# Kernel tuning notes

Measured on AMD Instinct MI355X. Metric: run time of the kernel, lower is better.

The kernel has to match this reference:

```python
import jax, jax.numpy as jnp
import numpy as np

# Problem sizes: batch(+heads), seq (m=n), head dim, nonzeros per row
B, M, N, K, R = 8, 4096, 4096, 64, 128
NNZ = M * R


def setup_inputs() -> dict:
    key = jax.random.key(0)
    k1, k2, k3, k4 = jax.random.split(key, 4)
    # Uniform CSR: R nonzeros per row, columns sorted within each row.
    row_offsets = jnp.arange(M + 1, dtype=jnp.int32) * R
    column_indices = jax.random.randint(k4, (M, R), 0, N, dtype=jnp.int32)
    column_indices = jnp.sort(column_indices, axis=1).reshape(NNZ)
    # diffsort(row_offsets): row ids sorted by descending row length (load balancing,
    # does not affect the math).
    diffs = row_offsets[1:] - row_offsets[:-1]
    row_indices = jnp.argsort(-diffs).astype(jnp.int32)
    q3d = jax.random.normal(k1, (B, M, K), dtype=jnp.float32)
    k3d = jax.random.normal(k2, (B, N, K), dtype=jnp.float32)
    v3d = jax.random.normal(k3, (B, N, K), dtype=jnp.float32)
    # `values` is only an output buffer for sddmm in the original; contents unused.
    values = jnp.zeros((B, NNZ), dtype=jnp.float32)
    return {
        "row_indices": row_indices,
        "row_offsets": row_offsets,
        "column_indices": column_indices,
        "q3d": q3d,
        "k3d": k3d,
        "v3d": v3d,
        "values": values,
    }


def reference(row_indices, row_offsets, column_indices, q3d, k3d, v3d, values):
    m = row_offsets.shape[0] - 1
    nnz = column_indices.shape[0]
    # Row id of each CSR nonzero.
    row_ids = jnp.searchsorted(
        row_offsets, jnp.arange(nnz, dtype=row_offsets.dtype), side="right"
    ) - 1
    cols = column_indices

    # SDDMM: logits[b, e] = <Q[b, row(e), :], K[b, col(e), :]>  -> [B, nnz]
    logits = jnp.einsum("bed,bed->be", q3d[:, row_ids, :], k3d[:, cols, :])

    def attend_one(lg_b, v_b):
        # Sparse per-row softmax over the nonzeros of each row.
        mx = jax.ops.segment_max(lg_b, row_ids, num_segments=m)
        ex = jnp.exp(lg_b - mx[row_ids])
        den = jax.ops.segment_sum(ex, row_ids, num_segments=m)
        w = ex / den[row_ids]  # [nnz]
        # SPMM: out[i, :] = sum_{e in row i} w[e] * V[col(e), :]
        return jax.ops.segment_sum(w[:, None] * v_b[cols, :], row_ids, num_segments=m)

    return jax.vmap(attend_one)(logits, v3d)  # [B, M, K]
```

## Files before the change

### kernel.cpp

```cpp
#include <hip/hip_runtime.h>

#define Bc 8
#define Mc 4096
#define Nc 4096
#define Kc 64
#define Rc 128

typedef _Float16 h16;
typedef h16 h16x2 __attribute__((ext_vector_type(2)));
typedef h16 h16x4 __attribute__((ext_vector_type(4)));
typedef h16 h16x8 __attribute__((ext_vector_type(8)));

__global__ __launch_bounds__(256) void cvt_fp16(
    const float4* __restrict__ K4, const float4* __restrict__ V4,
    h16x4* __restrict__ Kh4, h16x4* __restrict__ Vh4)
{
    const int n4 = Bc * Nc * Kc / 4;
    int i = blockIdx.x * 256 + threadIdx.x;
    const float4* src; h16x4* dst; int idx;
    if (i < n4) { src = K4; dst = Kh4; idx = i; }
    else        { src = V4; dst = Vh4; idx = i - n4; }
    float4 v = src[idx];
    h16x4 o = { (h16)v.x, (h16)v.y, (h16)v.z, (h16)v.w };
    dst[idx] = o;
}

__global__ __launch_bounds__(256) void sattn_kernel(
    const int* __restrict__ cols,
    const float* __restrict__ Q,
    const h16* __restrict__ Kh,
    const h16* __restrict__ Vh,
    float* __restrict__ out)
{
    const int b   = blockIdx.x & 7;
    const int row = blockIdx.x >> 3;
    const int t   = threadIdx.x;
    const int g   = t >> 3;
    const int ln  = t & 7;

    __shared__ float s_w[Rc];
    __shared__ __align__(16) float s_part[32][Kc];
    __shared__ __align__(16) float s_red[4][Kc];
    __shared__ float s_invden;

    int col4[4];
    #pragma unroll
    for (int p = 0; p < 4; ++p) col4[p] = cols[row * Rc + p * 32 + g];

    const float4* qp = (const float4*)(Q + (((unsigned)b * Mc + row) << 6) + ln * 8);
    float4 q0 = qp[0], q1 = qp[1];
    h16x2 qh[4];
    qh[0] = h16x2{ (h16)q0.x, (h16)q0.y };
    qh[1] = h16x2{ (h16)q0.z, (h16)q0.w };
    qh[2] = h16x2{ (h16)q1.x, (h16)q1.y };
    qh[3] = h16x2{ (h16)q1.z, (h16)q1.w };

    h16x8 kv[4];
    #pragma unroll
    for (int p = 0; p < 4; ++p)
        kv[p] = *(const h16x8*)(Kh + ((((unsigned)b * Nc + col4[p]) << 6) + ln * 8));

    #pragma unroll
    for (int p = 0; p < 4; ++p) {
        float acc = 0.f;
        #pragma unroll
        for (int j = 0; j < 4; ++j) {
            h16x2 kj = { kv[p][2 * j], kv[p][2 * j + 1] };
#if defined(__has_builtin)
#if __has_builtin(__builtin_amdgcn_fdot2)
            acc = __builtin_amdgcn_fdot2(qh[j], kj, acc, false);
#else
            acc += (float)qh[j].x * (float)kj.x + (float)qh[j].y * (float)kj.y;
#endif
#else
            acc += (float)qh[j].x * (float)kj.x + (float)qh[j].y * (float)kj.y;
#endif
        }
        acc += __shfl_xor(acc, 1, 64);
        acc += __shfl_xor(acc, 2, 64);
        acc += __shfl_xor(acc, 4, 64);
        if (ln == 0) s_w[p * 32 + g] = acc;
    }

    h16x8 vv[4];
    #pragma unroll
    for (int p = 0; p < 4; ++p)
        vv[p] = *(const h16x8*)(Vh + ((((unsigned)b * Nc + col4[p]) << 6) + ln * 8));

    __syncthreads();

    if (t < 64) {
        float l0 = s_w[t], l1 = s_w[t + 64];
        float m = fmaxf(l0, l1);
        #pragma unroll
        for (int o = 32; o; o >>= 1) m = fmaxf(m, __shfl_xor(m, o, 64));
        float e0 = __expf(l0 - m), e1 = __expf(l1 - m);
        s_w[t] = e0; s_w[t + 64] = e1;
        float s = e0 + e1;
        #pragma unroll
        for (int o = 32; o; o >>= 1) s += __shfl_xor(s, o, 64);
        if (t == 0) s_invden = 1.0f / s;
    }
    __syncthreads();

    float acc8[8] = {0.f,0.f,0.f,0.f,0.f,0.f,0.f,0.f};
    #pragma unroll
    for (int p = 0; p < 4; ++p) {
        const float w = s_w[p * 32 + g];
        #pragma unroll
        for (int j = 0; j < 8; ++j)
            acc8[j] = fmaf((float)vv[p][j], w, acc8[j]);
    }
    *(float4*)&s_part[g][ln * 8]     = *(float4*)&acc8[0];
    *(float4*)&s_part[g][ln * 8 + 4] = *(float4*)&acc8[4];
    __syncthreads();

    {
        const int k = t & 63, qq = t >> 6;
        float r = 0.f;
        #pragma unroll
        for (int j = 0; j < 8; ++j) r += s_part[qq * 8 + j][k];
        s_red[qq][k] = r;
    }
    __syncthreads();
    if (t < 64) {
        float r = (s_red[0][t] + s_red[1][t]) + (s_red[2][t] + s_red[3][t]);
        out[(((unsigned)b * Mc + row) << 6) + t] = r * s_invden;
    }
}

extern "C" void kernel_launch(void* const* d_in, const int* in_sizes, int n_in,
                              void* d_out, int out_size, void* d_ws, size_t ws_size,
                              hipStream_t stream) {
    const int*   cols = (const int*)d_in[2];
    const float* Q    = (const float*)d_in[3];
    const float* Km   = (const float*)d_in[4];
    const float* Vm   = (const float*)d_in[5];
    float* out = (float*)d_out;

    h16* Kh = (h16*)d_ws;
    h16* Vh = Kh + (size_t)Bc * Nc * Kc;

    const int n4 = Bc * Nc * Kc / 4;
    cvt_fp16<<<dim3(2 * n4 / 256), dim3(256), 0, stream>>>(
        (const float4*)Km, (const float4*)Vm, (h16x4*)Kh, (h16x4*)Vh);
    sattn_kernel<<<dim3(Bc * Mc), dim3(256), 0, stream>>>(cols, Q, Kh, Vh, out);
}
```

Measured before the change: 148.0 us.

## Process one row per wavefront and drop shared-memory reductions

Result: slower. 154.1 us (+4.1%).

```diff
diff --git a/kernel.cpp b/kernel.cpp
--- a/kernel.cpp
+++ b/kernel.cpp
@@ -10,122 +10,123 @@
 typedef h16 h16x2 __attribute__((ext_vector_type(2)));
 typedef h16 h16x4 __attribute__((ext_vector_type(4)));
 typedef h16 h16x8 __attribute__((ext_vector_type(8)));
+typedef float f32x4 __attribute__((ext_vector_type(4)));
 
 __global__ __launch_bounds__(256) void cvt_fp16(
-    const float4* __restrict__ K4, const float4* __restrict__ V4,
-    h16x4* __restrict__ Kh4, h16x4* __restrict__ Vh4)
+    const f32x4* __restrict__ K4, const f32x4* __restrict__ V4,
+    const f32x4* __restrict__ Q4,
+    h16x4* __restrict__ Kh4, h16x4* __restrict__ Vh4, h16x4* __restrict__ Qh4)
 {
-    const int n4 = Bc * Nc * Kc / 4;
-    int i = blockIdx.x * 256 + threadIdx.x;
-    const float4* src; h16x4* dst; int idx;
-    if (i < n4) { src = K4; dst = Kh4; idx = i; }
-    else        { src = V4; dst = Vh4; idx = i - n4; }
-    float4 v = src[idx];
+    const int nb4   = Nc * Kc / 4;
+    const int b     = blockIdx.x & 7;
+    const int chunk = blockIdx.x >> 3;
+    const int tsel  = chunk >> 8;
+    const int idx   = b * nb4 + ((chunk & 255) << 8) + threadIdx.x;
+    const f32x4* src = (tsel == 0) ? K4 : (tsel == 1) ? V4 : Q4;
+    h16x4*       dst = (tsel == 0) ? Kh4 : (tsel == 1) ? Vh4 : Qh4;
+    f32x4 v = __builtin_nontemporal_load(&src[idx]);
     h16x4 o = { (h16)v.x, (h16)v.y, (h16)v.z, (h16)v.w };
     dst[idx] = o;
 }
 
-__global__ __launch_bounds__(256) void sattn_kernel(
+__global__ __launch_bounds__(256, 4) void sattn_kernel(
     const int* __restrict__ cols,
-    const float* __restrict__ Q,
+    const h16* __restrict__ Qh,
     const h16* __restrict__ Kh,
     const h16* __restrict__ Vh,
     float* __restrict__ out)
 {
     const int b   = blockIdx.x & 7;
-    const int row = blockIdx.x >> 3;
-    const int t   = threadIdx.x;
-    const int g   = t >> 3;
-    const int ln  = t & 7;
+    const int w   = threadIdx.x >> 6;
+    const int row = ((blockIdx.x >> 3) << 2) | w;
+    const int l   = threadIdx.x & 63;
+    const int g   = l >> 3;
+    const int ln  = l & 7;
 
-    __shared__ float s_w[Rc];
-    __shared__ __align__(16) float s_part[32][Kc];
-    __shared__ __align__(16) float s_red[4][Kc];
-    __shared__ float s_invden;
+    const h16* Kb = Kh + ((size_t)b * Nc) * Kc;
+    const h16* Vb = Vh + ((size_t)b * Nc) * Kc;
 
-    int col4[4];
+    h16x8 qv = __builtin_nontemporal_load(
+        (const h16x8*)(Qh + (((size_t)b * Mc + row) << 6) + ln * 8));
+
+    const int* crow = cols + row * Rc;
+    int col16[16];
     #pragma unroll
-    for (int p = 0; p < 4; ++p) col4[p] = cols[row * Rc + p * 32 + g];
+    for (int p = 0; p < 16; ++p)
+        col16[p] = __builtin_nontemporal_load(&crow[p * 8 + g]);
 
-    const float4* qp = (const float4*)(Q + (((unsigned)b * Mc + row) << 6) + ln * 8);
-    float4 q0 = qp[0], q1 = qp[1];
-    h16x2 qh[4];
-    qh[0] = h16x2{ (h16)q0.x, (h16)q0.y };
-    qh[1] = h16x2{ (h16)q0.z, (h16)q0.w };
-    qh[2] = h16x2{ (h16)q1.x, (h16)q1.y };
-    qh[3] = h16x2{ (h16)q1.z, (h16)q1.w };
+    h16x8 kv[16];
+    #pragma unroll
+    for (int p = 0; p < 16; ++p)
+        kv[p] = *(const h16x8*)(Kb + (((unsigned)col16[p]) << 6) + ln * 8);
 
-    h16x8 kv[4];
+    float lg[16];
     #pragma unroll
-    for (int p = 0; p < 4; ++p)
-        kv[p] = *(const h16x8*)(Kh + ((((unsigned)b * Nc + col4[p]) << 6) + ln * 8));
-
-    #pragma unroll
-    for (int p = 0; p < 4; ++p) {
+    for (int p = 0; p < 16; ++p) {
         float acc = 0.f;
         #pragma unroll
         for (int j = 0; j < 4; ++j) {
+            h16x2 qj = { qv[2 * j], qv[2 * j + 1] };
             h16x2 kj = { kv[p][2 * j], kv[p][2 * j + 1] };
 #if defined(__has_builtin)
 #if __has_builtin(__builtin_amdgcn_fdot2)
-            acc = __builtin_amdgcn_fdot2(qh[j], kj, acc, false);
+            acc = __builtin_amdgcn_fdot2(qj, kj, acc, false);
 #else
-            acc += (float)qh[j].x * (float)kj.x + (float)qh[j].y * (float)kj.y;
+            acc += (float)qj.x * (float)kj.x + (float)qj.y * (float)kj.y;
 #endif
 #else
-            acc += (float)qh[j].x * (float)kj.x + (float)qh[j].y * (float)kj.y;
+            acc += (float)qj.x * (float)kj.x + (float)qj.y * (float)kj.y;
 #endif
         }
         acc += __shfl_xor(acc, 1, 64);
         acc += __shfl_xor(acc, 2, 64);
         acc += __shfl_xor(acc, 4, 64);
-        if (ln == 0) s_w[p * 32 + g] = acc;
+        lg[p] = acc;
     }
 
-    h16x8 vv[4];
+    h16x8 vv[16];
     #pragma unroll
-    for (int p = 0; p < 4; ++p)
-        vv[p] = *(const h16x8*)(Vh + ((((unsigned)b * Nc + col4[p]) << 6) + ln * 8));
+    for (int p = 0; p < 16; ++p)
+        vv[p] = *(const h16x8*)(Vb + (((unsigned)col16[p]) << 6) + ln * 8);
 
-    __syncthreads();
+    float m = lg[0];
+    #pragma unroll
+    for (int p = 1; p < 16; ++p) m = fmaxf(m, lg[p]);
+    m = fmaxf(m, __shfl_xor(m, 8, 64));
+    m = fmaxf(m, __shfl_xor(m, 16, 64));
+    m = fmaxf(m, __shfl_xor(m, 32, 64));
 
-    if (t < 64) {
-        float l0 = s_w[t], l1 = s_w[t + 64];
-        float m = fmaxf(l0, l1);
-        #pragma unroll
-        for (int o = 32; o; o >>= 1) m = fmaxf(m, __shfl_xor(m, o, 64));
-        float e0 = __expf(l0 - m), e1 = __expf(l1 - m);
-        s_w[t] = e0; s_w[t + 64] = e1;
-        float s = e0 + e1;
-        #pragma unroll
-        for (int o = 32; o; o >>= 1) s += __shfl_xor(s, o, 64);
-        if (t == 0) s_invden = 1.0f / s;
-    }
-    __syncthreads();
+    float e[16];
+    float s = 0.f;
+    #pragma unroll
+    for (int p = 0; p < 16; ++p) { e[p] = __expf(lg[p] - m); s += e[p]; }
+    s += __shfl_xor(s, 8, 64);
+    s += __shfl_xor(s, 16, 64);
+    s += __shfl_xor(s, 32, 64);
+    const float inv = 1.0f / s;
 
-    float acc8[8] = {0.f,0.f,0.f,0.f,0.f,0.f,0.f,0.f};
+    float acc8[8] = {0.f, 0.f, 0.f, 0.f, 0.f, 0.f, 0.f, 0.f};
     #pragma unroll
-    for (int p = 0; p < 4; ++p) {
-        const float w = s_w[p * 32 + g];
+    for (int p = 0; p < 16; ++p) {
+        const float wp = e[p];
         #pragma unroll
         for (int j = 0; j < 8; ++j)
-            acc8[j] = fmaf((float)vv[p][j], w, acc8[j]);
+            acc8[j] = fmaf((float)vv[p][j], wp, acc8[j]);
     }
-    *(float4*)&s_part[g][ln * 8]     = *(float4*)&acc8[0];
-    *(float4*)&s_part[g][ln * 8 + 4] = *(float4*)&acc8[4];
-    __syncthreads();
 
-    {
-        const int k = t & 63, qq = t >> 6;
-        float r = 0.f;
-        #pragma unroll
-        for (int j = 0; j < 8; ++j) r += s_part[qq * 8 + j][k];
-        s_red[qq][k] = r;
+    #pragma unroll
+    for (int j = 0; j < 8; ++j) {
+        acc8[j] += __shfl_xor(acc8[j], 8, 64);
+        acc8[j] += __shfl_xor(acc8[j], 16, 64);
+        acc8[j] += __shfl_xor(acc8[j], 32, 64);
     }
-    __syncthreads();
-    if (t < 64) {
-        float r = (s_red[0][t] + s_red[1][t]) + (s_red[2][t] + s_red[3][t]);
-        out[(((unsigned)b * Mc + row) << 6) + t] = r * s_invden;
+
+    if (g == 0) {
+        float* orow = out + (((size_t)b * Mc + row) << 6) + ln * 8;
+        f32x4 o0 = { acc8[0] * inv, acc8[1] * inv, acc8[2] * inv, acc8[3] * inv };
+        f32x4 o1 = { acc8[4] * inv, acc8[5] * inv, acc8[6] * inv, acc8[7] * inv };
+        __builtin_nontemporal_store(o0, (f32x4*)orow);
+        __builtin_nontemporal_store(o1, (f32x4*)orow + 1);
     }
 }
 
@@ -133,16 +134,18 @@
                               void* d_out, int out_size, void* d_ws, size_t ws_size,
                               hipStream_t stream) {
     const int*   cols = (const int*)d_in[2];
-    const float* Q    = (const float*)d_in[3];
+    const float* Qm   = (const float*)d_in[3];
     const float* Km   = (const float*)d_in[4];
     const float* Vm   = (const float*)d_in[5];
     float* out = (float*)d_out;
 
     h16* Kh = (h16*)d_ws;
     h16* Vh = Kh + (size_t)Bc * Nc * Kc;
+    h16* Qh = Vh + (size_t)Bc * Nc * Kc;
 
-    const int n4 = Bc * Nc * Kc / 4;
-    cvt_fp16<<<dim3(2 * n4 / 256), dim3(256), 0, stream>>>(
-        (const float4*)Km, (const float4*)Vm, (h16x4*)Kh, (h16x4*)Vh);
-    sattn_kernel<<<dim3(Bc * Mc), dim3(256), 0, stream>>>(cols, Q, Kh, Vh, out);
+    cvt_fp16<<<dim3(Bc * 3 * 256), dim3(256), 0, stream>>>(
+        (const f32x4*)Km, (const f32x4*)Vm, (const f32x4*)Qm,
+        (h16x4*)Kh, (h16x4*)Vh, (h16x4*)Qh);
+
+    sattn_kernel<<<dim3(Bc * Mc / 4), dim3(256), 0, stream>>>(cols, Qh, Kh, Vh, out);
 }
```
